# Kernel optimization log

Measured on AMD Instinct MI355X. Metric: run time of the kernel, lower is better.

Reference implementation:

```python
import jax, jax.numpy as jnp
import numpy as np

T, H, NH, NKV, HD, E, K, I = 1024, 2048, 16, 4, 128, 16, 2, 768
EPS = 1e-6
THETA = 10000.0


def setup_inputs() -> dict:
    key = jax.random.key(0)
    ks = jax.random.split(key, 8)
    s = 0.02
    return {
        "hidden_states": jax.random.normal(ks[0], (T, H), jnp.float32),
        "positions": jnp.arange(T, dtype=jnp.int32),
        "w_norm1": jnp.ones((H,), jnp.float32),
        "w_norm2": jnp.ones((H,), jnp.float32),
        "w_qkv": jax.random.normal(ks[1], (H, (NH + 2 * NKV) * HD), jnp.float32) * s,
        "w_qnorm": jnp.ones((HD,), jnp.float32),
        "w_knorm": jnp.ones((HD,), jnp.float32),
        "w_o": jax.random.normal(ks[2], (NH * HD, H), jnp.float32) * s,
        "w_router": jax.random.normal(ks[3], (H, E), jnp.float32) * s,
        "w_gate": jax.random.normal(ks[4], (E, H, I), jnp.float32) * s,
        "w_up": jax.random.normal(ks[5], (E, H, I), jnp.float32) * s,
        "w_down": jax.random.normal(ks[6], (E, I, H), jnp.float32) * s,
    }


def rmsnorm(x, w):
    return x * jax.lax.rsqrt(jnp.mean(x * x, axis=-1, keepdims=True) + EPS) * w


def apply_rope(x, positions):
    # NEOX-style rotary, full head_dim. x: [T, n_heads, HD]
    half = HD // 2
    inv_freq = 1.0 / (THETA ** (jnp.arange(half, dtype=jnp.float32) / half))
    ang = positions.astype(jnp.float32)[:, None] * inv_freq  # [T, half]
    cos = jnp.cos(ang)[:, None, :]
    sin = jnp.sin(ang)[:, None, :]
    x1, x2 = x[..., :half], x[..., half:]
    return jnp.concatenate([x1 * cos - x2 * sin, x2 * cos + x1 * sin], axis=-1)


def reference(hidden_states, positions, w_norm1, w_norm2, w_qkv, w_qnorm, w_knorm,
              w_o, w_router, w_gate, w_up, w_down):
    # prepare_attn: residual = x; h = input_layernorm(x)
    residual = hidden_states
    h = rmsnorm(hidden_states, w_norm1)

    # --- attention (bidirectional, GQA, per-head q/k RMSNorm + RoPE) ---
    qkv = h @ w_qkv
    q, k, v = jnp.split(qkv, [NH * HD, NH * HD + NKV * HD], axis=-1)
    q = rmsnorm(q.reshape(T, NH, HD), w_qnorm)
    k = rmsnorm(k.reshape(T, NKV, HD), w_knorm)
    v = v.reshape(T, NKV, HD)
    q = apply_rope(q, positions)
    k = apply_rope(k, positions)
    rep = NH // NKV
    kf = jnp.repeat(k, rep, axis=1)  # [T, NH, HD]
    vf = jnp.repeat(v, rep, axis=1)
    scores = jnp.einsum('tnd,snd->nts', q, kf) * (HD ** -0.5)  # [NH, T, T]
    p = jax.nn.softmax(scores, axis=-1)
    ctx = jnp.einsum('nts,snd->tnd', p, vf).reshape(T, NH * HD)
    attn_out = ctx @ w_o

    # prepare_mlp: residual = residual + attn_out; h = post_attention_layernorm(residual)
    residual = residual + attn_out
    h = rmsnorm(residual, w_norm2)

    # --- sparse MoE: softmax router, top-k renormalize, SwiGLU experts ---
    logits = h @ w_router
    probs = jax.nn.softmax(logits, axis=-1)
    topw, topi = jax.lax.top_k(probs, K)
    topw = topw / jnp.sum(topw, axis=-1, keepdims=True)
    gates = jnp.zeros((T, E), h.dtype).at[jnp.arange(T)[:, None], topi].set(topw)
    g = jnp.einsum('th,ehi->eti', h, w_gate)
    u = jnp.einsum('th,ehi->eti', h, w_up)
    y = jnp.einsum('eti,eih->eth', jax.nn.silu(g) * u, w_down)
    moe_out = jnp.einsum('eth,te->th', y, gates)

    return moe_out, residual
```

## Files before the change

### kernel.cpp

```cpp
#include <hip/hip_runtime.h>

#define T_    1024
#define H_    2048
#define NH_   16
#define NKV_  4
#define HD_   128
#define E_    16
#define I_    768
#define QKVN  3072

typedef __attribute__((ext_vector_type(8))) short  short8;
typedef __attribute__((ext_vector_type(4))) float  f32x4;
typedef unsigned short u16;

#define LDP 40

__device__ inline u16 f2bf(float f) {
  unsigned u = __builtin_bit_cast(unsigned, f);
  return (u16)((u + 0x7fffu + ((u >> 16) & 1u)) >> 16);
}
__device__ inline float bf2f(u16 h) {
  unsigned u = ((unsigned)h) << 16;
  return __builtin_bit_cast(float, u);
}

__device__ inline float blk_sum(float v, float* lds) {
#pragma unroll
  for (int o = 32; o; o >>= 1) v += __shfl_down(v, o);
  int w = threadIdx.x >> 6;
  __syncthreads();
  if ((threadIdx.x & 63) == 0) lds[w] = v;
  __syncthreads();
  float s = lds[0];
  int nw = blockDim.x >> 6;
  for (int i = 1; i < nw; ++i) s += lds[i];
  return s;
}
__device__ inline float blk_max(float v, float* lds) {
#pragma unroll
  for (int o = 32; o; o >>= 1) v = fmaxf(v, __shfl_down(v, o));
  int w = threadIdx.x >> 6;
  __syncthreads();
  if ((threadIdx.x & 63) == 0) lds[w] = v;
  __syncthreads();
  float s = lds[0];
  int nw = blockDim.x >> 6;
  for (int i = 1; i < nw; ++i) s = fmaxf(s, lds[i]);
  return s;
}


struct AU4 { uint4 v; };
struct BU2 { uint2 v; };
struct F4  { float v[4]; };

__device__ inline void wrS(u16* lds, const AU4& r) {
  *(uint4*)(lds + (threadIdx.x >> 2) * LDP + (threadIdx.x & 3) * 8) = r.v;
}
__device__ inline void wrS(u16* lds, const BU2& r) {
  *(uint2*)(lds + (threadIdx.x >> 3) * LDP + (threadIdx.x & 7) * 4) = r.v;
}
__device__ inline void wrS(u16* lds, const F4& r) {
  int n = threadIdx.x & 63, kh = (threadIdx.x >> 6) * 4;
  uint2 w;
  w.x = (unsigned)f2bf(r.v[0]) | ((unsigned)f2bf(r.v[1]) << 16);
  w.y = (unsigned)f2bf(r.v[2]) | ((unsigned)f2bf(r.v[3]) << 16);
  *(uint2*)(lds + n * LDP + kh) = w;
}

__device__ inline void mma2(const u16* As, const u16* Bs, f32x4 acc[2][2]) {
  const int lane = threadIdx.x & 63, wv = threadIdx.x >> 6;
  const int wr = wv >> 1, wc = wv & 1;
  const int kk = (lane >> 4) * 8, rr = lane & 15;
  short8 aF[2], bF[2];
#pragma unroll
  for (int m = 0; m < 2; ++m)
    aF[m] = *(const short8*)(As + (wr * 32 + m * 16 + rr) * LDP + kk);
#pragma unroll
  for (int n = 0; n < 2; ++n)
    bF[n] = *(const short8*)(Bs + (wc * 32 + n * 16 + rr) * LDP + kk);
#pragma unroll
  for (int m = 0; m < 2; ++m)
#pragma unroll
    for (int n = 0; n < 2; ++n)
      acc[m][n] = __builtin_amdgcn_mfma_f32_16x16x32_bf16(aF[m], bF[n], acc[m][n], 0, 0, 0);
}

#define ZERO_ACC(acc) do { \
  _Pragma("unroll") for (int m_ = 0; m_ < 2; ++m_) \
  _Pragma("unroll") for (int n_ = 0; n_ < 2; ++n_) acc[m_][n_] = (f32x4){0.f,0.f,0.f,0.f}; \
} while (0)

#define EPI_ROW(m, r)  (((threadIdx.x >> 6) >> 1) * 32 + (m)*16 + (((threadIdx.x&63) >> 4) * 4) + (r))
#define EPI_COL(n)     ((((threadIdx.x >> 6) & 1) * 32) + (n)*16 + ((threadIdx.x&63) & 15))

template<int NT, class AT, class BT, class LA, class LB>
__device__ inline void pipe2(LA la, LB lb, u16* A0, u16* B0, u16* A1, u16* B1,
                             f32x4 acc[2][2]) {
  AT a0, a1; BT b0, b1;
  la(a0, 0); lb(b0, 0);
  la(a1, 1); lb(b1, 1);
  wrS(A0, a0); wrS(B0, b0);
  if (NT > 2) { la(a0, 2); lb(b0, 2); }
#pragma unroll 1
  for (int kt = 0; kt < NT; kt += 2) {
    __syncthreads();
    wrS(A1, a1); wrS(B1, b1);
    if (kt + 3 < NT) { la(a1, kt + 3); lb(b1, kt + 3); }
    mma2(A0, B0, acc);
    __syncthreads();
    if (kt + 2 < NT) { wrS(A0, a0); wrS(B0, b0); }
    if (kt + 4 < NT) { la(a0, kt + 4); lb(b0, kt + 4); }
    mma2(A1, B1, acc);
  }
}


__global__ __launch_bounds__(256) void k_rms1(const float* x, const float* w, u16* out) {
  __shared__ float lds[4];
  int t = blockIdx.x, tid = threadIdx.x;
  float v[8]; float ss = 0.f;
#pragma unroll
  for (int i = 0; i < 8; ++i) { v[i] = x[(size_t)t * H_ + tid + 256 * i]; ss += v[i] * v[i]; }
  ss = blk_sum(ss, lds);
  float inv = rsqrtf(ss * (1.f / H_) + 1e-6f);
#pragma unroll
  for (int i = 0; i < 8; ++i)
    out[(size_t)t * H_ + tid + 256 * i] = f2bf(v[i] * inv * w[tid + 256 * i]);
}

__global__ __launch_bounds__(256) void k_rms2(const float* x, const float* w,
                                              float* outf, u16* outb) {
  __shared__ float lds[4];
  int t = blockIdx.x, tid = threadIdx.x;
  float v[8]; float ss = 0.f;
#pragma unroll
  for (int i = 0; i < 8; ++i) { v[i] = x[(size_t)t * H_ + tid + 256 * i]; ss += v[i] * v[i]; }
  ss = blk_sum(ss, lds);
  float inv = rsqrtf(ss * (1.f / H_) + 1e-6f);
#pragma unroll
  for (int i = 0; i < 8; ++i) {
    float r = v[i] * inv * w[tid + 256 * i];
    outf[(size_t)t * H_ + tid + 256 * i] = r;
    outb[(size_t)t * H_ + tid + 256 * i] = f2bf(r);
  }
}

__global__ __launch_bounds__(512) void k_qkv(const u16* h1, const float* wqkv, float* qkv) {
  __shared__ __align__(16) u16 A0[128 * LDP], B0[64 * LDP], A1[128 * LDP], B1[64 * LDP];
  int bn = blockIdx.x, bm = blockIdx.y;
  f32x4 acc[2][2]; ZERO_ACC(acc);
  auto la = [&](AU4& r, int kt) {
    r.v = *(const uint4*)(h1 + (size_t)(bm * 128 + (threadIdx.x >> 2)) * H_ + kt * 32 + (threadIdx.x & 3) * 8);
  };
  auto lb = [&](F4& r, int kt) {
    int n = threadIdx.x & 63, kh = (threadIdx.x >> 6) * 4;
    const float* src = wqkv + (size_t)(kt * 32 + kh) * QKVN + bn * 64 + n;
#pragma unroll
    for (int j = 0; j < 4; ++j) r.v[j] = src[(size_t)j * QKVN];
  };
  pipe2<H_ / 32, AU4, F4>(la, lb, A0, B0, A1, B1, acc);
#pragma unroll
  for (int m = 0; m < 2; ++m)
#pragma unroll
    for (int n = 0; n < 2; ++n) {
      f32x4 a = acc[m][n];
#pragma unroll
      for (int r = 0; r < 4; ++r)
        qkv[(size_t)(bm * 128 + EPI_ROW(m, r)) * QKVN + bn * 64 + EPI_COL(n)] = a[r];
    }
}

__global__ __launch_bounds__(256) void k_qkrope(const float* qkv, const int* pos,
                                                const float* wq, const float* wk,
                                                u16* q, u16* kk, u16* vT) {
  __shared__ float cs[64], sn[64];
  int t = blockIdx.x, tid = threadIdx.x, lane = tid & 63, w = tid >> 6;
  if (tid < 64) {
    float fr = expf(-((float)tid / 64.f) * 9.210340371976184f);
    float ang = (float)pos[t] * fr;
    float s_, c_; sincosf(ang, &s_, &c_);
    cs[tid] = c_; sn[tid] = s_;
  }
  __syncthreads();
  const float* row = qkv + (size_t)t * QKVN;
  for (int h = w; h < NH_; h += 4) {
    float x1 = row[h * 128 + lane], x2 = row[h * 128 + 64 + lane];
    float ss = x1 * x1 + x2 * x2;
#pragma unroll
    for (int o = 32; o; o >>= 1) ss += __shfl_down(ss, o);
    ss = __shfl(ss, 0);
    float inv = rsqrtf(ss * (1.f / HD_) + 1e-6f);
    float n1 = x1 * inv * wq[lane], n2 = x2 * inv * wq[64 + lane];
    float o1 = n1 * cs[lane] - n2 * sn[lane];
    float o2 = n2 * cs[lane] + n1 * sn[lane];
    q[(size_t)t * (NH_ * HD_) + h * 128 + lane] = f2bf(o1);
    q[(size_t)t * (NH_ * HD_) + h * 128 + 64 + lane] = f2bf(o2);
  }
  if (w < NKV_) {
    int h = w;
    float x1 = row[2048 + h * 128 + lane], x2 = row[2048 + h * 128 + 64 + lane];
    float ss = x1 * x1 + x2 * x2;
#pragma unroll
    for (int o = 32; o; o >>= 1) ss += __shfl_down(ss, o);
    ss = __shfl(ss, 0);
    float inv = rsqrtf(ss * (1.f / HD_) + 1e-6f);
    float n1 = x1 * inv * wk[lane], n2 = x2 * inv * wk[64 + lane];
    float o1 = n1 * cs[lane] - n2 * sn[lane];
    float o2 = n2 * cs[lane] + n1 * sn[lane];
    kk[((size_t)h * T_ + t) * HD_ + lane] = f2bf(o1);
    kk[((size_t)h * T_ + t) * HD_ + 64 + lane] = f2bf(o2);
    float v1 = row[2560 + h * 128 + lane], v2 = row[2560 + h * 128 + 64 + lane];
    vT[((size_t)(h * 128 + lane)) * T_ + t] = f2bf(v1);
    vT[((size_t)(h * 128 + 64 + lane)) * T_ + t] = f2bf(v2);
  }
}

__global__ __launch_bounds__(512) void k_scores(const u16* q, const u16* kb, u16* S) {
  __shared__ __align__(16) u16 A0[128 * LDP], B0[64 * LDP], A1[128 * LDP], B1[64 * LDP];
  int h = blockIdx.x, sn = blockIdx.y, qm = blockIdx.z;
  const u16* Aq = q + h * 128;
  const u16* Bk = kb + (size_t)(h >> 2) * T_ * HD_;
  f32x4 acc[2][2]; ZERO_ACC(acc);
  auto la = [&](AU4& r, int kt) {
    r.v = *(const uint4*)(Aq + (size_t)(qm * 128 + (threadIdx.x >> 2)) * (NH_ * HD_) + kt * 32 + (threadIdx.x & 3) * 8);
  };
  auto lb = [&](BU2& r, int kt) {
    r.v = *(const uint2*)(Bk + (size_t)(sn * 64 + (threadIdx.x >> 3)) * HD_ + kt * 32 + (threadIdx.x & 7) * 4);
  };
  pipe2<HD_ / 32, AU4, BU2>(la, lb, A0, B0, A1, B1, acc);
  const float scale = 0.08838834764831845f;
#pragma unroll
  for (int m = 0; m < 2; ++m)
#pragma unroll
    for (int n = 0; n < 2; ++n) {
      f32x4 a = acc[m][n];
#pragma unroll
      for (int r = 0; r < 4; ++r)
        S[((size_t)h * T_ + qm * 128 + EPI_ROW(m, r)) * T_ + sn * 64 + EPI_COL(n)] =
            f2bf(a[r] * scale);
    }
}

__global__ __launch_bounds__(256) void k_softmax(u16* S) {
  __shared__ float lds[4];
  int t = blockIdx.x, h = blockIdx.y, tid = threadIdx.x;
  u16* rowp = S + ((size_t)h * T_ + t) * T_;
  float x[4];
#pragma unroll
  for (int i = 0; i < 4; ++i) x[i] = bf2f(rowp[tid + 256 * i]);
  float m = fmaxf(fmaxf(x[0], x[1]), fmaxf(x[2], x[3]));
  m = blk_max(m, lds);
  float s = 0.f;
#pragma unroll
  for (int i = 0; i < 4; ++i) { x[i] = __expf(x[i] - m); s += x[i]; }
  s = blk_sum(s, lds);
  float inv = 1.f / s;
#pragma unroll
  for (int i = 0; i < 4; ++i) rowp[tid + 256 * i] = f2bf(x[i] * inv);
}

__global__ __launch_bounds__(512) void k_pv(const u16* P, const u16* vT, u16* ctx) {
  __shared__ __align__(16) u16 A0[128 * LDP], B0[64 * LDP], A1[128 * LDP], B1[64 * LDP];
  int h = blockIdx.x, qm = blockIdx.y, nb = blockIdx.z;
  const u16* Ap = P + (size_t)h * T_ * T_;
  const u16* Bv = vT + (size_t)(h >> 2) * HD_ * T_ + (size_t)nb * 64 * T_;
  f32x4 acc[2][2]; ZERO_ACC(acc);
  auto la = [&](AU4& r, int kt) {
    r.v = *(const uint4*)(Ap + (size_t)(qm * 128 + (threadIdx.x >> 2)) * T_ + kt * 32 + (threadIdx.x & 3) * 8);
  };
  auto lb = [&](BU2& r, int kt) {
    r.v = *(const uint2*)(Bv + (size_t)(threadIdx.x >> 3) * T_ + kt * 32 + (threadIdx.x & 7) * 4);
  };
  pipe2<T_ / 32, AU4, BU2>(la, lb, A0, B0, A1, B1, acc);
#pragma unroll
  for (int m = 0; m < 2; ++m)
#pragma unroll
    for (int n = 0; n < 2; ++n) {
      f32x4 a = acc[m][n];
#pragma unroll
      for (int r = 0; r < 4; ++r)
        ctx[(size_t)(qm * 128 + EPI_ROW(m, r)) * (NH_ * HD_) + h * 128 + nb * 64 + EPI_COL(n)] =
            f2bf(a[r]);
    }
}

__global__ __launch_bounds__(512) void k_wo(const u16* ctx, const float* wo,
                                            const float* hs, float* resid) {
  __shared__ __align__(16) u16 A0[128 * LDP], B0[64 * LDP], A1[128 * LDP], B1[64 * LDP];
  int bn = blockIdx.x, bm = blockIdx.y;
  f32x4 acc[2][2]; ZERO_ACC(acc);
  auto la = [&](AU4& r, int kt) {
    r.v = *(const uint4*)(ctx + (size_t)(bm * 128 + (threadIdx.x >> 2)) * H_ + kt * 32 + (threadIdx.x & 3) * 8);
  };
  auto lb = [&](F4& r, int kt) {
    int n = threadIdx.x & 63, kh = (threadIdx.x >> 6) * 4;
    const float* src = wo + (size_t)(kt * 32 + kh) * H_ + bn * 64 + n;
#pragma unroll
    for (int j = 0; j < 4; ++j) r.v[j] = src[(size_t)j * H_];
  };
  pipe2<H_ / 32, AU4, F4>(la, lb, A0, B0, A1, B1, acc);
#pragma unroll
  for (int m = 0; m < 2; ++m)
#pragma unroll
    for (int n = 0; n < 2; ++n) {
      f32x4 a = acc[m][n];
#pragma unroll
      for (int r = 0; r < 4; ++r) {
        size_t idx = (size_t)(bm * 128 + EPI_ROW(m, r)) * H_ + bn * 64 + EPI_COL(n);
        resid[idx] = a[r] + hs[idx];
      }
    }
}

__global__ __launch_bounds__(256) void k_router(const float* h2f, const float* wr_,
                                                int* topi, float* topw, int* cnt) {
  __shared__ float xs[H_];
  __shared__ float red[4][16];
  __shared__ float lg[16];
  int t = blockIdx.x, tid = threadIdx.x;
#pragma unroll
  for (int i = 0; i < 8; ++i) xs[tid + 256 * i] = h2f[(size_t)t * H_ + tid + 256 * i];
  __syncthreads();
  int e = tid & 15, p = tid >> 4;
  float s = 0.f;
  int b0 = p * 128;
  for (int i = 0; i < 128; ++i) s += xs[b0 + i] * wr_[(size_t)(b0 + i) * E_ + e];
  s += __shfl_down(s, 32);
  s += __shfl_down(s, 16);
  int lane = tid & 63, w = tid >> 6;
  if (lane < 16) red[w][lane] = s;
  __syncthreads();
  if (tid < 16) lg[tid] = red[0][tid] + red[1][tid] + red[2][tid] + red[3][tid];
  __syncthreads();
  if (tid == 0) {
    float l1 = -1e30f; int e1 = 0;
    for (int i = 0; i < E_; ++i) if (lg[i] > l1) { l1 = lg[i]; e1 = i; }
    float l2 = -1e30f; int e2 = 0;
    for (int i = 0; i < E_; ++i) if (i != e1 && lg[i] > l2) { l2 = lg[i]; e2 = i; }
    float d = __expf(l2 - l1);
    float w1 = 1.f / (1.f + d), w2 = d / (1.f + d);
    topi[2 * t] = e1; topi[2 * t + 1] = e2;
    topw[2 * t] = w1; topw[2 * t + 1] = w2;
    atomicAdd(&cnt[e1], 1);
    atomicAdd(&cnt[e2], 1);
  }
}

__global__ void k_scan(const int* cnt, int* basearr) {
  if (threadIdx.x == 0) {
    int b = 0;
    for (int e = 0; e < E_; ++e) { basearr[e] = b; b += cnt[e]; }
    basearr[E_] = b;
  }
}

__global__ __launch_bounds__(256) void k_assign(const int* topi, const float* topw,
                                                const int* basearr, int* posc,
                                                int* tok, float* wslot) {
  int t = blockIdx.x * 256 + threadIdx.x;
  if (t < T_) {
#pragma unroll
    for (int j = 0; j < 2; ++j) {
      int e = topi[2 * t + j];
      int p = atomicAdd(&posc[e], 1);
      int s = basearr[e] + p;
      tok[s] = t;
      wslot[s] = topw[2 * t + j];
    }
  }
}

__global__ __launch_bounds__(512) void k_gateup(const u16* h2b,
                                                const float* wg, const float* wu,
                                                const int* cnt, const int* basearr, const int* tok,
                                                u16* act) {
  __shared__ __align__(16) u16 A0[128 * LDP], B0[64 * LDP], A1[128 * LDP], B1[64 * LDP];
  __shared__ int gat_s[128];
  int e = blockIdx.x;
  int c = cnt[e];
  int mt = blockIdx.z;
  if (mt * 128 >= c) return;
  int basee = basearr[e];
  int gmax = c - mt * 128;
  int n0 = blockIdx.y * 32;
  int tid = threadIdx.x;
  if (tid < 128) {
    int r = mt * 128 + tid;
    gat_s[tid] = (r < c) ? tok[basee + r] : tok[basee];
  }
  __syncthreads();
  const float* Bg = wg + (size_t)e * H_ * I_;
  const float* Bu = wu + (size_t)e * H_ * I_;
  f32x4 acc[2][2]; ZERO_ACC(acc);
  auto la = [&](AU4& r, int kt) {
    r.v = *(const uint4*)(h2b + (size_t)gat_s[threadIdx.x >> 2] * H_ + kt * 32 + (threadIdx.x & 3) * 8);
  };
  auto lb = [&](F4& r, int kt) {
    int cidx = threadIdx.x & 63, kh = (threadIdx.x >> 6) * 4;
    int fn = cidx >> 4;
    const float* base = (fn & 1) ? Bu : Bg;
    int col = n0 + (fn >> 1) * 16 + (cidx & 15);
    const float* src = base + (size_t)(kt * 32 + kh) * I_ + col;
#pragma unroll
    for (int j = 0; j < 4; ++j) r.v[j] = src[(size_t)j * I_];
  };
  pipe2<H_ / 32, AU4, F4>(la, lb, A0, B0, A1, B1, acc);
  int slot0 = basee + mt * 128;
  int col = n0 + ((threadIdx.x >> 6) & 1) * 16 + ((threadIdx.x & 63) & 15);
#pragma unroll
  for (int m = 0; m < 2; ++m) {
#pragma unroll
    for (int r = 0; r < 4; ++r) {
      int row = EPI_ROW(m, r);
      if (row >= gmax) continue;
      float g = acc[m][0][r], u = acc[m][1][r];
      float sg = g / (1.f + __expf(-g));
      act[(size_t)(slot0 + row) * I_ + col] = f2bf(sg * u);
    }
  }
}

__global__ __launch_bounds__(512) void k_down(const u16* act, const float* wd,
                                              const int* cnt, const int* basearr,
                                              const int* tok, const float* wslot,
                                              float* moe) {
  __shared__ __align__(16) u16 A0[128 * LDP], B0[64 * LDP], A1[128 * LDP], B1[64 * LDP];
  int e = blockIdx.y;
  int c = cnt[e];
  int mt = blockIdx.z;
  if (mt * 128 >= c) return;
  int basee = basearr[e];
  int gmax = c - mt * 128;
  int slot0 = basee + mt * 128;
  int n0 = blockIdx.x * 64;
  const u16* Ap = act + (size_t)slot0 * I_;
  const float* Bp = wd + (size_t)e * I_ * H_;
  f32x4 acc[2][2]; ZERO_ACC(acc);
  auto la = [&](AU4& r, int kt) {
    r.v = *(const uint4*)(Ap + (size_t)(threadIdx.x >> 2) * I_ + kt * 32 + (threadIdx.x & 3) * 8);
  };
  auto lb = [&](F4& r, int kt) {
    int n = threadIdx.x & 63, kh = (threadIdx.x >> 6) * 4;
    const float* src = Bp + (size_t)(kt * 32 + kh) * H_ + n0 + n;
#pragma unroll
    for (int j = 0; j < 4; ++j) r.v[j] = src[(size_t)j * H_];
  };
  pipe2<I_ / 32, AU4, F4>(la, lb, A0, B0, A1, B1, acc);
#pragma unroll
  for (int m = 0; m < 2; ++m)
#pragma unroll
    for (int n = 0; n < 2; ++n) {
      f32x4 a = acc[m][n];
#pragma unroll
      for (int r = 0; r < 4; ++r) {
        int row = EPI_ROW(m, r);
        if (row >= gmax) continue;
        int col = EPI_COL(n);
        int slot = slot0 + row;
        float wgt = wslot[slot];
        int tk = tok[slot];
        atomicAdd(&moe[(size_t)tk * H_ + n0 + col], a[r] * wgt);
      }
    }
}

extern "C" void kernel_launch(void* const* d_in, const int* in_sizes, int n_in,
                              void* d_out, int out_size, void* d_ws, size_t ws_size,
                              hipStream_t stream) {
  const float* hs    = (const float*)d_in[0];
  const int*   pos   = (const int*)d_in[1];
  const float* wn1   = (const float*)d_in[2];
  const float* wn2   = (const float*)d_in[3];
  const float* wqkv  = (const float*)d_in[4];
  const float* wqn   = (const float*)d_in[5];
  const float* wkn   = (const float*)d_in[6];
  const float* wo    = (const float*)d_in[7];
  const float* wrt   = (const float*)d_in[8];
  const float* wg    = (const float*)d_in[9];
  const float* wu    = (const float*)d_in[10];
  const float* wd    = (const float*)d_in[11];
  float* out = (float*)d_out;
  float* moe_out = out;
  float* resid   = out + (size_t)T_ * H_;

  char* ws = (char*)d_ws;
  size_t off = 0;
  auto alloc = [&](size_t bytes) { size_t r = off; off = (off + bytes + 255) & ~(size_t)255; return r; };
  u16*   h1   = (u16*)  (ws + alloc((size_t)T_ * H_ * 2));
  float* qkv  = (float*)(ws + alloc((size_t)T_ * QKVN * 4));
  u16*   q    = (u16*)  (ws + alloc((size_t)T_ * NH_ * HD_ * 2));
  u16*   kb   = (u16*)  (ws + alloc((size_t)NKV_ * T_ * HD_ * 2));
  u16*   vT   = (u16*)  (ws + alloc((size_t)NKV_ * HD_ * T_ * 2));
  u16*   S    = (u16*)  (ws + alloc((size_t)NH_ * T_ * T_ * 2));
  u16*   ctx  = (u16*)  (ws + alloc((size_t)T_ * NH_ * HD_ * 2));
  float* h2f  = (float*)(ws + alloc((size_t)T_ * H_ * 4));
  u16*   h2b  = (u16*)  (ws + alloc((size_t)T_ * H_ * 2));
  u16*   act  = (u16*)  (ws + alloc((size_t)(2 * T_ + 256) * I_ * 2));
  int*   topi = (int*)  (ws + alloc((size_t)T_ * 2 * 4));
  float* topw = (float*)(ws + alloc((size_t)T_ * 2 * 4));
  int*   cnt  = (int*)  (ws + alloc(32 * 4));
  int*   posc = cnt + 16;
  int*   base = (int*)  (ws + alloc(32 * 4));
  int*   tok  = (int*)  (ws + alloc((size_t)(2 * T_ + 128) * 4));
  float* wsl  = (float*)(ws + alloc((size_t)(2 * T_ + 128) * 4));
  (void)ws_size; (void)in_sizes; (void)n_in; (void)out_size;

  hipMemsetAsync(moe_out, 0, (size_t)T_ * H_ * 4, stream);
  hipMemsetAsync(cnt, 0, 32 * 4, stream);

  k_rms1<<<T_, 256, 0, stream>>>(hs, wn1, h1);
  k_qkv<<<dim3(QKVN / 64, T_ / 128), 512, 0, stream>>>(h1, wqkv, qkv);
  k_qkrope<<<T_, 256, 0, stream>>>(qkv, pos, wqn, wkn, q, kb, vT);
  k_scores<<<dim3(NH_, T_ / 64, T_ / 128), 512, 0, stream>>>(q, kb, S);
  k_softmax<<<dim3(T_, NH_), 256, 0, stream>>>(S);
  k_pv<<<dim3(NH_, T_ / 128, HD_ / 64), 512, 0, stream>>>(S, vT, ctx);
  k_wo<<<dim3(H_ / 64, T_ / 128), 512, 0, stream>>>(ctx, wo, hs, resid);
  k_rms2<<<T_, 256, 0, stream>>>(resid, wn2, h2f, h2b);
  k_router<<<T_, 256, 0, stream>>>(h2f, wrt, topi, topw, cnt);
  k_scan<<<1, 64, 0, stream>>>(cnt, base);
  k_assign<<<4, 256, 0, stream>>>(topi, topw, base, posc, tok, wsl);
  k_gateup<<<dim3(E_, I_ / 32, T_ / 128), 512, 0, stream>>>(h2b, wg, wu, cnt, base, tok, act);
  k_down<<<dim3(H_ / 64, E_, T_ / 128), 512, 0, stream>>>(act, wd, cnt, base, tok, wsl, moe_out);
}
```

Before: 341.5 us.

## Load GEMM operand tiles directly into LDS and shrink tiles to 64 rows

Every MFMA GEMM kernel now stages its bf16 A tile, and for attention also the B tile, with global_load_lds, writing straight from global memory into LDS instead of going through registers. The A tiles use an unpadded 32-element row stride to match the per-wave DMA layout. Block tiles shrink from 128x64 with 512 threads to 64x64 with 256 threads, and fp32 weight B loads now take 8 rows per thread. The aim is fewer register round trips and more blocks in flight. The cost is that fp32 weights are re-read by twice as many M tiles, and the unpadded LDS layout may cause bank conflicts.

```diff
diff --git a/kernel.cpp b/kernel.cpp
--- a/kernel.cpp
+++ b/kernel.cpp
@@ -13,7 +13,8 @@
 typedef __attribute__((ext_vector_type(4))) float  f32x4;
 typedef unsigned short u16;
 
-#define LDP 40
+#define LDPA 32
+#define LDPB 40
 
 __device__ inline u16 f2bf(float f) {
   unsigned u = __builtin_bit_cast(unsigned, f);
@@ -22,6 +23,12 @@
 __device__ inline float bf2f(u16 h) {
   unsigned u = ((unsigned)h) << 16;
   return __builtin_bit_cast(float, u);
+}
+
+__device__ inline void gll16(const u16* g, u16* l) {
+  __builtin_amdgcn_global_load_lds(
+      (const __attribute__((address_space(1))) void*)g,
+      (__attribute__((address_space(3))) void*)l, 16, 0, 0);
 }
 
 __device__ inline float blk_sum(float v, float* lds) {
@@ -50,24 +57,19 @@
 }
 
 
-struct AU4 { uint4 v; };
-struct BU2 { uint2 v; };
-struct F4  { float v[4]; };
-
-__device__ inline void wrS(u16* lds, const AU4& r) {
-  *(uint4*)(lds + (threadIdx.x >> 2) * LDP + (threadIdx.x & 3) * 8) = r.v;
-}
-__device__ inline void wrS(u16* lds, const BU2& r) {
-  *(uint2*)(lds + (threadIdx.x >> 3) * LDP + (threadIdx.x & 7) * 4) = r.v;
-}
-__device__ inline void wrS(u16* lds, const F4& r) {
-  int n = threadIdx.x & 63, kh = (threadIdx.x >> 6) * 4;
-  uint2 w;
+struct F8 { float v[8]; };
+
+__device__ inline void wrB(u16* lds, const F8& r) {
+  int n = threadIdx.x & 63, kh = (threadIdx.x >> 6) * 8;
+  uint4 w;
   w.x = (unsigned)f2bf(r.v[0]) | ((unsigned)f2bf(r.v[1]) << 16);
   w.y = (unsigned)f2bf(r.v[2]) | ((unsigned)f2bf(r.v[3]) << 16);
-  *(uint2*)(lds + n * LDP + kh) = w;
-}
-
+  w.z = (unsigned)f2bf(r.v[4]) | ((unsigned)f2bf(r.v[5]) << 16);
+  w.w = (unsigned)f2bf(r.v[6]) | ((unsigned)f2bf(r.v[7]) << 16);
+  *(uint4*)(lds + n * LDPB + kh) = w;
+}
+
+template<int SA, int SB>
 __device__ inline void mma2(const u16* As, const u16* Bs, f32x4 acc[2][2]) {
   const int lane = threadIdx.x & 63, wv = threadIdx.x >> 6;
   const int wr = wv >> 1, wc = wv & 1;
@@ -75,10 +77,10 @@
   short8 aF[2], bF[2];
 #pragma unroll
   for (int m = 0; m < 2; ++m)
-    aF[m] = *(const short8*)(As + (wr * 32 + m * 16 + rr) * LDP + kk);
+    aF[m] = *(const short8*)(As + (wr * 32 + m * 16 + rr) * SA + kk);
 #pragma unroll
   for (int n = 0; n < 2; ++n)
-    bF[n] = *(const short8*)(Bs + (wc * 32 + n * 16 + rr) * LDP + kk);
+    bF[n] = *(const short8*)(Bs + (wc * 32 + n * 16 + rr) * SB + kk);
 #pragma unroll
   for (int m = 0; m < 2; ++m)
 #pragma unroll
@@ -94,24 +96,40 @@
 #define EPI_ROW(m, r)  (((threadIdx.x >> 6) >> 1) * 32 + (m)*16 + (((threadIdx.x&63) >> 4) * 4) + (r))
 #define EPI_COL(n)     ((((threadIdx.x >> 6) & 1) * 32) + (n)*16 + ((threadIdx.x&63) & 15))
 
-template<int NT, class AT, class BT, class LA, class LB>
-__device__ inline void pipe2(LA la, LB lb, u16* A0, u16* B0, u16* A1, u16* B1,
+template<int NT, class GA, class LB>
+__device__ inline void pipeF(GA gllA, LB ldB, u16* A0, u16* B0, u16* A1, u16* B1,
                              f32x4 acc[2][2]) {
-  AT a0, a1; BT b0, b1;
-  la(a0, 0); lb(b0, 0);
-  la(a1, 1); lb(b1, 1);
-  wrS(A0, a0); wrS(B0, b0);
-  if (NT > 2) { la(a0, 2); lb(b0, 2); }
+  F8 b0, b1;
+  gllA(A0, 0);
+  ldB(b0, 0); ldB(b1, 1);
+  wrB(B0, b0);
+  if (NT > 2) ldB(b0, 2);
 #pragma unroll 1
   for (int kt = 0; kt < NT; kt += 2) {
     __syncthreads();
-    wrS(A1, a1); wrS(B1, b1);
-    if (kt + 3 < NT) { la(a1, kt + 3); lb(b1, kt + 3); }
-    mma2(A0, B0, acc);
+    gllA(A1, kt + 1);
+    wrB(B1, b1);
+    if (kt + 3 < NT) ldB(b1, kt + 3);
+    mma2<LDPA, LDPB>(A0, B0, acc);
     __syncthreads();
-    if (kt + 2 < NT) { wrS(A0, a0); wrS(B0, b0); }
-    if (kt + 4 < NT) { la(a0, kt + 4); lb(b0, kt + 4); }
-    mma2(A1, B1, acc);
+    if (kt + 2 < NT) { gllA(A0, kt + 2); wrB(B0, b0); }
+    if (kt + 4 < NT) ldB(b0, kt + 4);
+    mma2<LDPA, LDPB>(A1, B1, acc);
+  }
+}
+
+template<int NT, class GA, class GB>
+__device__ inline void pipeG(GA gllA, GB gllB, u16* A0, u16* B0, u16* A1, u16* B1,
+                             f32x4 acc[2][2]) {
+  gllA(A0, 0); gllB(B0, 0);
+#pragma unroll 1
+  for (int kt = 0; kt < NT; kt += 2) {
+    __syncthreads();
+    gllA(A1, kt + 1); gllB(B1, kt + 1);
+    mma2<LDPA, LDPA>(A0, B0, acc);
+    __syncthreads();
+    if (kt + 2 < NT) { gllA(A0, kt + 2); gllB(B0, kt + 2); }
+    mma2<LDPA, LDPA>(A1, B1, acc);
   }
 }
 
@@ -146,20 +164,22 @@
   }
 }
 
-__global__ __launch_bounds__(512) void k_qkv(const u16* h1, const float* wqkv, float* qkv) {
-  __shared__ __align__(16) u16 A0[128 * LDP], B0[64 * LDP], A1[128 * LDP], B1[64 * LDP];
+__global__ __launch_bounds__(256) void k_qkv(const u16* h1, const float* wqkv, float* qkv) {
+  __shared__ __align__(16) u16 A0[64 * LDPA], A1[64 * LDPA];
+  __shared__ __align__(16) u16 B0[64 * LDPB], B1[64 * LDPB];
   int bn = blockIdx.x, bm = blockIdx.y;
   f32x4 acc[2][2]; ZERO_ACC(acc);
-  auto la = [&](AU4& r, int kt) {
-    r.v = *(const uint4*)(h1 + (size_t)(bm * 128 + (threadIdx.x >> 2)) * H_ + kt * 32 + (threadIdx.x & 3) * 8);
-  };
-  auto lb = [&](F4& r, int kt) {
-    int n = threadIdx.x & 63, kh = (threadIdx.x >> 6) * 4;
+  auto la = [&](u16* As, int kt) {
+    gll16(h1 + (size_t)(bm * 64 + (threadIdx.x >> 2)) * H_ + kt * 32 + (threadIdx.x & 3) * 8,
+          As + (threadIdx.x & 192) * 8);
+  };
+  auto lb = [&](F8& r, int kt) {
+    int n = threadIdx.x & 63, kh = (threadIdx.x >> 6) * 8;
     const float* src = wqkv + (size_t)(kt * 32 + kh) * QKVN + bn * 64 + n;
 #pragma unroll
-    for (int j = 0; j < 4; ++j) r.v[j] = src[(size_t)j * QKVN];
-  };
-  pipe2<H_ / 32, AU4, F4>(la, lb, A0, B0, A1, B1, acc);
+    for (int j = 0; j < 8; ++j) r.v[j] = src[(size_t)j * QKVN];
+  };
+  pipeF<H_ / 32>(la, lb, A0, B0, A1, B1, acc);
 #pragma unroll
   for (int m = 0; m < 2; ++m)
 #pragma unroll
@@ -167,7 +187,7 @@
       f32x4 a = acc[m][n];
 #pragma unroll
       for (int r = 0; r < 4; ++r)
-        qkv[(size_t)(bm * 128 + EPI_ROW(m, r)) * QKVN + bn * 64 + EPI_COL(n)] = a[r];
+        qkv[(size_t)(bm * 64 + EPI_ROW(m, r)) * QKVN + bn * 64 + EPI_COL(n)] = a[r];
     }
 }
 
@@ -216,19 +236,22 @@
   }
 }
 
-__global__ __launch_bounds__(512) void k_scores(const u16* q, const u16* kb, u16* S) {
-  __shared__ __align__(16) u16 A0[128 * LDP], B0[64 * LDP], A1[128 * LDP], B1[64 * LDP];
+__global__ __launch_bounds__(256) void k_scores(const u16* q, const u16* kb, u16* S) {
+  __shared__ __align__(16) u16 A0[64 * LDPA], A1[64 * LDPA];
+  __shared__ __align__(16) u16 B0[64 * LDPA], B1[64 * LDPA];
   int h = blockIdx.x, sn = blockIdx.y, qm = blockIdx.z;
   const u16* Aq = q + h * 128;
   const u16* Bk = kb + (size_t)(h >> 2) * T_ * HD_;
   f32x4 acc[2][2]; ZERO_ACC(acc);
-  auto la = [&](AU4& r, int kt) {
-    r.v = *(const uint4*)(Aq + (size_t)(qm * 128 + (threadIdx.x >> 2)) * (NH_ * HD_) + kt * 32 + (threadIdx.x & 3) * 8);
-  };
-  auto lb = [&](BU2& r, int kt) {
-    r.v = *(const uint2*)(Bk + (size_t)(sn * 64 + (threadIdx.x >> 3)) * HD_ + kt * 32 + (threadIdx.x & 7) * 4);
-  };
-  pipe2<HD_ / 32, AU4, BU2>(la, lb, A0, B0, A1, B1, acc);
+  auto la = [&](u16* As, int kt) {
+    gll16(Aq + (size_t)(qm * 64 + (threadIdx.x >> 2)) * (NH_ * HD_) + kt * 32 + (threadIdx.x & 3) * 8,
+          As + (threadIdx.x & 192) * 8);
+  };
+  auto lb = [&](u16* Bs, int kt) {
+    gll16(Bk + (size_t)(sn * 64 + (threadIdx.x >> 2)) * HD_ + kt * 32 + (threadIdx.x & 3) * 8,
+          Bs + (threadIdx.x & 192) * 8);
+  };
+  pipeG<HD_ / 32>(la, lb, A0, B0, A1, B1, acc);
   const float scale = 0.08838834764831845f;
 #pragma unroll
   for (int m = 0; m < 2; ++m)
@@ -237,7 +260,7 @@
       f32x4 a = acc[m][n];
 #pragma unroll
       for (int r = 0; r < 4; ++r)
-        S[((size_t)h * T_ + qm * 128 + EPI_ROW(m, r)) * T_ + sn * 64 + EPI_COL(n)] =
+        S[((size_t)h * T_ + qm * 64 + EPI_ROW(m, r)) * T_ + sn * 64 + EPI_COL(n)] =
             f2bf(a[r] * scale);
     }
 }
@@ -260,19 +283,22 @@
   for (int i = 0; i < 4; ++i) rowp[tid + 256 * i] = f2bf(x[i] * inv);
 }
 
-__global__ __launch_bounds__(512) void k_pv(const u16* P, const u16* vT, u16* ctx) {
-  __shared__ __align__(16) u16 A0[128 * LDP], B0[64 * LDP], A1[128 * LDP], B1[64 * LDP];
+__global__ __launch_bounds__(256) void k_pv(const u16* P, const u16* vT, u16* ctx) {
+  __shared__ __align__(16) u16 A0[64 * LDPA], A1[64 * LDPA];
+  __shared__ __align__(16) u16 B0[64 * LDPA], B1[64 * LDPA];
   int h = blockIdx.x, qm = blockIdx.y, nb = blockIdx.z;
   const u16* Ap = P + (size_t)h * T_ * T_;
   const u16* Bv = vT + (size_t)(h >> 2) * HD_ * T_ + (size_t)nb * 64 * T_;
   f32x4 acc[2][2]; ZERO_ACC(acc);
-  auto la = [&](AU4& r, int kt) {
-    r.v = *(const uint4*)(Ap + (size_t)(qm * 128 + (threadIdx.x >> 2)) * T_ + kt * 32 + (threadIdx.x & 3) * 8);
-  };
-  auto lb = [&](BU2& r, int kt) {
-    r.v = *(const uint2*)(Bv + (size_t)(threadIdx.x >> 3) * T_ + kt * 32 + (threadIdx.x & 7) * 4);
-  };
-  pipe2<T_ / 32, AU4, BU2>(la, lb, A0, B0, A1, B1, acc);
+  auto la = [&](u16* As, int kt) {
+    gll16(Ap + (size_t)(qm * 64 + (threadIdx.x >> 2)) * T_ + kt * 32 + (threadIdx.x & 3) * 8,
+          As + (threadIdx.x & 192) * 8);
+  };
+  auto lb = [&](u16* Bs, int kt) {
+    gll16(Bv + (size_t)(threadIdx.x >> 2) * T_ + kt * 32 + (threadIdx.x & 3) * 8,
+          Bs + (threadIdx.x & 192) * 8);
+  };
+  pipeG<T_ / 32>(la, lb, A0, B0, A1, B1, acc);
 #pragma unroll
   for (int m = 0; m < 2; ++m)
 #pragma unroll
@@ -280,26 +306,28 @@
       f32x4 a = acc[m][n];
 #pragma unroll
       for (int r = 0; r < 4; ++r)
-        ctx[(size_t)(qm * 128 + EPI_ROW(m, r)) * (NH_ * HD_) + h * 128 + nb * 64 + EPI_COL(n)] =
+        ctx[(size_t)(qm * 64 + EPI_ROW(m, r)) * (NH_ * HD_) + h * 128 + nb * 64 + EPI_COL(n)] =
             f2bf(a[r]);
     }
 }
 
-__global__ __launch_bounds__(512) void k_wo(const u16* ctx, const float* wo,
+__global__ __launch_bounds__(256) void k_wo(const u16* ctx, const float* wo,
                                             const float* hs, float* resid) {
-  __shared__ __align__(16) u16 A0[128 * LDP], B0[64 * LDP], A1[128 * LDP], B1[64 * LDP];
+  __shared__ __align__(16) u16 A0[64 * LDPA], A1[64 * LDPA];
+  __shared__ __align__(16) u16 B0[64 * LDPB], B1[64 * LDPB];
   int bn = blockIdx.x, bm = blockIdx.y;
   f32x4 acc[2][2]; ZERO_ACC(acc);
-  auto la = [&](AU4& r, int kt) {
-    r.v = *(const uint4*)(ctx + (size_t)(bm * 128 + (threadIdx.x >> 2)) * H_ + kt * 32 + (threadIdx.x & 3) * 8);
-  };
-  auto lb = [&](F4& r, int kt) {
-    int n = threadIdx.x & 63, kh = (threadIdx.x >> 6) * 4;
+  auto la = [&](u16* As, int kt) {
+    gll16(ctx + (size_t)(bm * 64 + (threadIdx.x >> 2)) * H_ + kt * 32 + (threadIdx.x & 3) * 8,
+          As + (threadIdx.x & 192) * 8);
+  };
+  auto lb = [&](F8& r, int kt) {
+    int n = threadIdx.x & 63, kh = (threadIdx.x >> 6) * 8;
     const float* src = wo + (size_t)(kt * 32 + kh) * H_ + bn * 64 + n;
 #pragma unroll
-    for (int j = 0; j < 4; ++j) r.v[j] = src[(size_t)j * H_];
-  };
-  pipe2<H_ / 32, AU4, F4>(la, lb, A0, B0, A1, B1, acc);
+    for (int j = 0; j < 8; ++j) r.v[j] = src[(size_t)j * H_];
+  };
+  pipeF<H_ / 32>(la, lb, A0, B0, A1, B1, acc);
 #pragma unroll
   for (int m = 0; m < 2; ++m)
 #pragma unroll
@@ -307,7 +335,7 @@
       f32x4 a = acc[m][n];
 #pragma unroll
       for (int r = 0; r < 4; ++r) {
-        size_t idx = (size_t)(bm * 128 + EPI_ROW(m, r)) * H_ + bn * 64 + EPI_COL(n);
+        size_t idx = (size_t)(bm * 64 + EPI_ROW(m, r)) * H_ + bn * 64 + EPI_COL(n);
         resid[idx] = a[r] + hs[idx];
       }
     }
@@ -371,43 +399,45 @@
   }
 }
 
-__global__ __launch_bounds__(512) void k_gateup(const u16* h2b,
+__global__ __launch_bounds__(256) void k_gateup(const u16* h2b,
                                                 const float* wg, const float* wu,
                                                 const int* cnt, const int* basearr, const int* tok,
                                                 u16* act) {
-  __shared__ __align__(16) u16 A0[128 * LDP], B0[64 * LDP], A1[128 * LDP], B1[64 * LDP];
-  __shared__ int gat_s[128];
+  __shared__ __align__(16) u16 A0[64 * LDPA], A1[64 * LDPA];
+  __shared__ __align__(16) u16 B0[64 * LDPB], B1[64 * LDPB];
+  __shared__ int gat_s[64];
   int e = blockIdx.x;
   int c = cnt[e];
   int mt = blockIdx.z;
-  if (mt * 128 >= c) return;
+  if (mt * 64 >= c) return;
   int basee = basearr[e];
-  int gmax = c - mt * 128;
+  int gmax = c - mt * 64;
   int n0 = blockIdx.y * 32;
   int tid = threadIdx.x;
-  if (tid < 128) {
-    int r = mt * 128 + tid;
+  if (tid < 64) {
+    int r = mt * 64 + tid;
     gat_s[tid] = (r < c) ? tok[basee + r] : tok[basee];
   }
   __syncthreads();
+  int grow = gat_s[tid >> 2];
   const float* Bg = wg + (size_t)e * H_ * I_;
   const float* Bu = wu + (size_t)e * H_ * I_;
   f32x4 acc[2][2]; ZERO_ACC(acc);
-  auto la = [&](AU4& r, int kt) {
-    r.v = *(const uint4*)(h2b + (size_t)gat_s[threadIdx.x >> 2] * H_ + kt * 32 + (threadIdx.x & 3) * 8);
-  };
-  auto lb = [&](F4& r, int kt) {
-    int cidx = threadIdx.x & 63, kh = (threadIdx.x >> 6) * 4;
+  auto la = [&](u16* As, int kt) {
+    gll16(h2b + (size_t)grow * H_ + kt * 32 + (tid & 3) * 8, As + (tid & 192) * 8);
+  };
+  auto lb = [&](F8& r, int kt) {
+    int cidx = tid & 63, kh = (tid >> 6) * 8;
     int fn = cidx >> 4;
     const float* base = (fn & 1) ? Bu : Bg;
     int col = n0 + (fn >> 1) * 16 + (cidx & 15);
     const float* src = base + (size_t)(kt * 32 + kh) * I_ + col;
 #pragma unroll
-    for (int j = 0; j < 4; ++j) r.v[j] = src[(size_t)j * I_];
-  };
-  pipe2<H_ / 32, AU4, F4>(la, lb, A0, B0, A1, B1, acc);
-  int slot0 = basee + mt * 128;
-  int col = n0 + ((threadIdx.x >> 6) & 1) * 16 + ((threadIdx.x & 63) & 15);
+    for (int j = 0; j < 8; ++j) r.v[j] = src[(size_t)j * I_];
+  };
+  pipeF<H_ / 32>(la, lb, A0, B0, A1, B1, acc);
+  int slot0 = basee + mt * 64;
+  int col = n0 + ((tid >> 6) & 1) * 16 + ((tid & 63) & 15);
 #pragma unroll
   for (int m = 0; m < 2; ++m) {
 #pragma unroll
@@ -421,32 +451,34 @@
   }
 }
 
-__global__ __launch_bounds__(512) void k_down(const u16* act, const float* wd,
+__global__ __launch_bounds__(256) void k_down(const u16* act, const float* wd,
                                               const int* cnt, const int* basearr,
                                               const int* tok, const float* wslot,
                                               float* moe) {
-  __shared__ __align__(16) u16 A0[128 * LDP], B0[64 * LDP], A1[128 * LDP], B1[64 * LDP];
+  __shared__ __align__(16) u16 A0[64 * LDPA], A1[64 * LDPA];
+  __shared__ __align__(16) u16 B0[64 * LDPB], B1[64 * LDPB];
   int e = blockIdx.y;
   int c = cnt[e];
   int mt = blockIdx.z;
-  if (mt * 128 >= c) return;
+  if (mt * 64 >= c) return;
   int basee = basearr[e];
-  int gmax = c - mt * 128;
-  int slot0 = basee + mt * 128;
+  int gmax = c - mt * 64;
+  int slot0 = basee + mt * 64;
   int n0 = blockIdx.x * 64;
   const u16* Ap = act + (size_t)slot0 * I_;
   const float* Bp = wd + (size_t)e * I_ * H_;
   f32x4 acc[2][2]; ZERO_ACC(acc);
-  auto la = [&](AU4& r, int kt) {
-    r.v = *(const uint4*)(Ap + (size_t)(threadIdx.x >> 2) * I_ + kt * 32 + (threadIdx.x & 3) * 8);
-  };
-  auto lb = [&](F4& r, int kt) {
-    int n = threadIdx.x & 63, kh = (threadIdx.x >> 6) * 4;
+  auto la = [&](u16* As, int kt) {
+    gll16(Ap + (size_t)(threadIdx.x >> 2) * I_ + kt * 32 + (threadIdx.x & 3) * 8,
+          As + (threadIdx.x & 192) * 8);
+  };
+  auto lb = [&](F8& r, int kt) {
+    int n = threadIdx.x & 63, kh = (threadIdx.x >> 6) * 8;
     const float* src = Bp + (size_t)(kt * 32 + kh) * H_ + n0 + n;
 #pragma unroll
-    for (int j = 0; j < 4; ++j) r.v[j] = src[(size_t)j * H_];
-  };
-  pipe2<I_ / 32, AU4, F4>(la, lb, A0, B0, A1, B1, acc);
+    for (int j = 0; j < 8; ++j) r.v[j] = src[(size_t)j * H_];
+  };
+  pipeF<I_ / 32>(la, lb, A0, B0, A1, B1, acc);
 #pragma unroll
   for (int m = 0; m < 2; ++m)
 #pragma unroll
@@ -510,16 +542,16 @@
   hipMemsetAsync(cnt, 0, 32 * 4, stream);
 
   k_rms1<<<T_, 256, 0, stream>>>(hs, wn1, h1);
-  k_qkv<<<dim3(QKVN / 64, T_ / 128), 512, 0, stream>>>(h1, wqkv, qkv);
+  k_qkv<<<dim3(QKVN / 64, T_ / 64), 256, 0, stream>>>(h1, wqkv, qkv);
   k_qkrope<<<T_, 256, 0, stream>>>(qkv, pos, wqn, wkn, q, kb, vT);
-  k_scores<<<dim3(NH_, T_ / 64, T_ / 128), 512, 0, stream>>>(q, kb, S);
+  k_scores<<<dim3(NH_, T_ / 64, T_ / 64), 256, 0, stream>>>(q, kb, S);
   k_softmax<<<dim3(T_, NH_), 256, 0, stream>>>(S);
-  k_pv<<<dim3(NH_, T_ / 128, HD_ / 64), 512, 0, stream>>>(S, vT, ctx);
-  k_wo<<<dim3(H_ / 64, T_ / 128), 512, 0, stream>>>(ctx, wo, hs, resid);
+  k_pv<<<dim3(NH_, T_ / 64, HD_ / 64), 256, 0, stream>>>(S, vT, ctx);
+  k_wo<<<dim3(H_ / 64, T_ / 64), 256, 0, stream>>>(ctx, wo, hs, resid);
   k_rms2<<<T_, 256, 0, stream>>>(resid, wn2, h2f, h2b);
   k_router<<<T_, 256, 0, stream>>>(h2f, wrt, topi, topw, cnt);
   k_scan<<<1, 64, 0, stream>>>(cnt, base);
   k_assign<<<4, 256, 0, stream>>>(topi, topw, base, posc, tok, wsl);
-  k_gateup<<<dim3(E_, I_ / 32, T_ / 128), 512, 0, stream>>>(h2b, wg, wu, cnt, base, tok, act);
-  k_down<<<dim3(H_ / 64, E_, T_ / 128), 512, 0, stream>>>(act, wd, cnt, base, tok, wsl, moe_out);
-}
+  k_gateup<<<dim3(E_, I_ / 32, T_ / 64), 256, 0, stream>>>(h2b, wg, wu, cnt, base, tok, act);
+  k_down<<<dim3(H_ / 64, E_, T_ / 64), 256, 0, stream>>>(act, wd, cnt, base, tok, wsl, moe_out);
+}
```

After: 360.7 us. +5.6%, slower.

## Split-K the QKV, O-proj, gate/up and down GEMMs with atomic accumulation

Applied to the files above, without the earlier changes.

Splits the K dimension in two for the QKV, Wo, gate/up and down projection GEMMs, doubling the grid and accumulating partial results with float atomicAdd into zeroed buffers. The residual add is replaced by pre-copying hidden_states into the output, and the SiLU*up epilogue moves into a separate k_silu kernel over fp32 partial buffers. The aim is more blocks to fill the GPU's compute units, since the base grids are small (e.g. 384 or 256 blocks). The cost is extra memsets, atomic traffic, larger fp32 intermediates and one extra launch.

```diff
diff --git a/kernel.cpp b/kernel.cpp
--- a/kernel.cpp
+++ b/kernel.cpp
@@ -148,18 +148,20 @@
 
 __global__ __launch_bounds__(512) void k_qkv(const u16* h1, const float* wqkv, float* qkv) {
   __shared__ __align__(16) u16 A0[128 * LDP], B0[64 * LDP], A1[128 * LDP], B1[64 * LDP];
-  int bn = blockIdx.x, bm = blockIdx.y;
+  int bn = blockIdx.x, bm = blockIdx.y, ks = blockIdx.z;
+  const u16* Ab = h1 + ks * (H_ / 2);
+  const float* Bb = wqkv + (size_t)ks * (H_ / 2) * QKVN;
   f32x4 acc[2][2]; ZERO_ACC(acc);
   auto la = [&](AU4& r, int kt) {
-    r.v = *(const uint4*)(h1 + (size_t)(bm * 128 + (threadIdx.x >> 2)) * H_ + kt * 32 + (threadIdx.x & 3) * 8);
+    r.v = *(const uint4*)(Ab + (size_t)(bm * 128 + (threadIdx.x >> 2)) * H_ + kt * 32 + (threadIdx.x & 3) * 8);
   };
   auto lb = [&](F4& r, int kt) {
     int n = threadIdx.x & 63, kh = (threadIdx.x >> 6) * 4;
-    const float* src = wqkv + (size_t)(kt * 32 + kh) * QKVN + bn * 64 + n;
+    const float* src = Bb + (size_t)(kt * 32 + kh) * QKVN + bn * 64 + n;
 #pragma unroll
     for (int j = 0; j < 4; ++j) r.v[j] = src[(size_t)j * QKVN];
   };
-  pipe2<H_ / 32, AU4, F4>(la, lb, A0, B0, A1, B1, acc);
+  pipe2<H_ / 64, AU4, F4>(la, lb, A0, B0, A1, B1, acc);
 #pragma unroll
   for (int m = 0; m < 2; ++m)
 #pragma unroll
@@ -167,7 +169,7 @@
       f32x4 a = acc[m][n];
 #pragma unroll
       for (int r = 0; r < 4; ++r)
-        qkv[(size_t)(bm * 128 + EPI_ROW(m, r)) * QKVN + bn * 64 + EPI_COL(n)] = a[r];
+        atomicAdd(&qkv[(size_t)(bm * 128 + EPI_ROW(m, r)) * QKVN + bn * 64 + EPI_COL(n)], a[r]);
     }
 }
 
@@ -285,31 +287,30 @@
     }
 }
 
-__global__ __launch_bounds__(512) void k_wo(const u16* ctx, const float* wo,
-                                            const float* hs, float* resid) {
+__global__ __launch_bounds__(512) void k_wo(const u16* ctx, const float* wo, float* resid) {
   __shared__ __align__(16) u16 A0[128 * LDP], B0[64 * LDP], A1[128 * LDP], B1[64 * LDP];
-  int bn = blockIdx.x, bm = blockIdx.y;
+  int bn = blockIdx.x, bm = blockIdx.y, ks = blockIdx.z;
+  const u16* Ab = ctx + ks * (H_ / 2);
+  const float* Bb = wo + (size_t)ks * (H_ / 2) * H_;
   f32x4 acc[2][2]; ZERO_ACC(acc);
   auto la = [&](AU4& r, int kt) {
-    r.v = *(const uint4*)(ctx + (size_t)(bm * 128 + (threadIdx.x >> 2)) * H_ + kt * 32 + (threadIdx.x & 3) * 8);
+    r.v = *(const uint4*)(Ab + (size_t)(bm * 128 + (threadIdx.x >> 2)) * H_ + kt * 32 + (threadIdx.x & 3) * 8);
   };
   auto lb = [&](F4& r, int kt) {
     int n = threadIdx.x & 63, kh = (threadIdx.x >> 6) * 4;
-    const float* src = wo + (size_t)(kt * 32 + kh) * H_ + bn * 64 + n;
+    const float* src = Bb + (size_t)(kt * 32 + kh) * H_ + bn * 64 + n;
 #pragma unroll
     for (int j = 0; j < 4; ++j) r.v[j] = src[(size_t)j * H_];
   };
-  pipe2<H_ / 32, AU4, F4>(la, lb, A0, B0, A1, B1, acc);
+  pipe2<H_ / 64, AU4, F4>(la, lb, A0, B0, A1, B1, acc);
 #pragma unroll
   for (int m = 0; m < 2; ++m)
 #pragma unroll
     for (int n = 0; n < 2; ++n) {
       f32x4 a = acc[m][n];
 #pragma unroll
-      for (int r = 0; r < 4; ++r) {
-        size_t idx = (size_t)(bm * 128 + EPI_ROW(m, r)) * H_ + bn * 64 + EPI_COL(n);
-        resid[idx] = a[r] + hs[idx];
-      }
+      for (int r = 0; r < 4; ++r)
+        atomicAdd(&resid[(size_t)(bm * 128 + EPI_ROW(m, r)) * H_ + bn * 64 + EPI_COL(n)], a[r]);
     }
 }
 
@@ -374,12 +375,12 @@
 __global__ __launch_bounds__(512) void k_gateup(const u16* h2b,
                                                 const float* wg, const float* wu,
                                                 const int* cnt, const int* basearr, const int* tok,
-                                                u16* act) {
+                                                float* gpart, float* upart) {
   __shared__ __align__(16) u16 A0[128 * LDP], B0[64 * LDP], A1[128 * LDP], B1[64 * LDP];
   __shared__ int gat_s[128];
   int e = blockIdx.x;
   int c = cnt[e];
-  int mt = blockIdx.z;
+  int mt = blockIdx.z >> 1, ks = blockIdx.z & 1;
   if (mt * 128 >= c) return;
   int basee = basearr[e];
   int gmax = c - mt * 128;
@@ -390,11 +391,12 @@
     gat_s[tid] = (r < c) ? tok[basee + r] : tok[basee];
   }
   __syncthreads();
-  const float* Bg = wg + (size_t)e * H_ * I_;
-  const float* Bu = wu + (size_t)e * H_ * I_;
+  const u16* Ab = h2b + ks * (H_ / 2);
+  const float* Bg = wg + (size_t)e * H_ * I_ + (size_t)ks * (H_ / 2) * I_;
+  const float* Bu = wu + (size_t)e * H_ * I_ + (size_t)ks * (H_ / 2) * I_;
   f32x4 acc[2][2]; ZERO_ACC(acc);
   auto la = [&](AU4& r, int kt) {
-    r.v = *(const uint4*)(h2b + (size_t)gat_s[threadIdx.x >> 2] * H_ + kt * 32 + (threadIdx.x & 3) * 8);
+    r.v = *(const uint4*)(Ab + (size_t)gat_s[threadIdx.x >> 2] * H_ + kt * 32 + (threadIdx.x & 3) * 8);
   };
   auto lb = [&](F4& r, int kt) {
     int cidx = threadIdx.x & 63, kh = (threadIdx.x >> 6) * 4;
@@ -405,7 +407,7 @@
 #pragma unroll
     for (int j = 0; j < 4; ++j) r.v[j] = src[(size_t)j * I_];
   };
-  pipe2<H_ / 32, AU4, F4>(la, lb, A0, B0, A1, B1, acc);
+  pipe2<H_ / 64, AU4, F4>(la, lb, A0, B0, A1, B1, acc);
   int slot0 = basee + mt * 128;
   int col = n0 + ((threadIdx.x >> 6) & 1) * 16 + ((threadIdx.x & 63) & 15);
 #pragma unroll
@@ -414,11 +416,25 @@
     for (int r = 0; r < 4; ++r) {
       int row = EPI_ROW(m, r);
       if (row >= gmax) continue;
-      float g = acc[m][0][r], u = acc[m][1][r];
-      float sg = g / (1.f + __expf(-g));
-      act[(size_t)(slot0 + row) * I_ + col] = f2bf(sg * u);
-    }
-  }
+      size_t idx = (size_t)(slot0 + row) * I_ + col;
+      atomicAdd(&gpart[idx], acc[m][0][r]);
+      atomicAdd(&upart[idx], acc[m][1][r]);
+    }
+  }
+}
+
+__global__ __launch_bounds__(256) void k_silu(const float* gpart, const float* upart, u16* act) {
+  int gid = blockIdx.x * 256 + threadIdx.x;
+  float4 g = ((const float4*)gpart)[gid];
+  float4 u = ((const float4*)upart)[gid];
+  float o0 = g.x / (1.f + __expf(-g.x)) * u.x;
+  float o1 = g.y / (1.f + __expf(-g.y)) * u.y;
+  float o2 = g.z / (1.f + __expf(-g.z)) * u.z;
+  float o3 = g.w / (1.f + __expf(-g.w)) * u.w;
+  uint2 w;
+  w.x = (unsigned)f2bf(o0) | ((unsigned)f2bf(o1) << 16);
+  w.y = (unsigned)f2bf(o2) | ((unsigned)f2bf(o3) << 16);
+  ((uint2*)act)[gid] = w;
 }
 
 __global__ __launch_bounds__(512) void k_down(const u16* act, const float* wd,
@@ -428,14 +444,14 @@
   __shared__ __align__(16) u16 A0[128 * LDP], B0[64 * LDP], A1[128 * LDP], B1[64 * LDP];
   int e = blockIdx.y;
   int c = cnt[e];
-  int mt = blockIdx.z;
+  int mt = blockIdx.z >> 1, ks = blockIdx.z & 1;
   if (mt * 128 >= c) return;
   int basee = basearr[e];
   int gmax = c - mt * 128;
   int slot0 = basee + mt * 128;
   int n0 = blockIdx.x * 64;
-  const u16* Ap = act + (size_t)slot0 * I_;
-  const float* Bp = wd + (size_t)e * I_ * H_;
+  const u16* Ap = act + (size_t)slot0 * I_ + ks * (I_ / 2);
+  const float* Bp = wd + (size_t)e * I_ * H_ + (size_t)ks * (I_ / 2) * H_;
   f32x4 acc[2][2]; ZERO_ACC(acc);
   auto la = [&](AU4& r, int kt) {
     r.v = *(const uint4*)(Ap + (size_t)(threadIdx.x >> 2) * I_ + kt * 32 + (threadIdx.x & 3) * 8);
@@ -446,7 +462,7 @@
 #pragma unroll
     for (int j = 0; j < 4; ++j) r.v[j] = src[(size_t)j * H_];
   };
-  pipe2<I_ / 32, AU4, F4>(la, lb, A0, B0, A1, B1, acc);
+  pipe2<I_ / 64, AU4, F4>(la, lb, A0, B0, A1, B1, acc);
 #pragma unroll
   for (int m = 0; m < 2; ++m)
 #pragma unroll
@@ -487,39 +503,46 @@
   char* ws = (char*)d_ws;
   size_t off = 0;
   auto alloc = [&](size_t bytes) { size_t r = off; off = (off + bytes + 255) & ~(size_t)255; return r; };
-  u16*   h1   = (u16*)  (ws + alloc((size_t)T_ * H_ * 2));
-  float* qkv  = (float*)(ws + alloc((size_t)T_ * QKVN * 4));
-  u16*   q    = (u16*)  (ws + alloc((size_t)T_ * NH_ * HD_ * 2));
-  u16*   kb   = (u16*)  (ws + alloc((size_t)NKV_ * T_ * HD_ * 2));
-  u16*   vT   = (u16*)  (ws + alloc((size_t)NKV_ * HD_ * T_ * 2));
-  u16*   S    = (u16*)  (ws + alloc((size_t)NH_ * T_ * T_ * 2));
-  u16*   ctx  = (u16*)  (ws + alloc((size_t)T_ * NH_ * HD_ * 2));
-  float* h2f  = (float*)(ws + alloc((size_t)T_ * H_ * 4));
-  u16*   h2b  = (u16*)  (ws + alloc((size_t)T_ * H_ * 2));
-  u16*   act  = (u16*)  (ws + alloc((size_t)(2 * T_ + 256) * I_ * 2));
-  int*   topi = (int*)  (ws + alloc((size_t)T_ * 2 * 4));
-  float* topw = (float*)(ws + alloc((size_t)T_ * 2 * 4));
-  int*   cnt  = (int*)  (ws + alloc(32 * 4));
-  int*   posc = cnt + 16;
-  int*   base = (int*)  (ws + alloc(32 * 4));
-  int*   tok  = (int*)  (ws + alloc((size_t)(2 * T_ + 128) * 4));
-  float* wsl  = (float*)(ws + alloc((size_t)(2 * T_ + 128) * 4));
+  u16*   h1    = (u16*)  (ws + alloc((size_t)T_ * H_ * 2));
+  float* qkv   = (float*)(ws + alloc((size_t)T_ * QKVN * 4));
+  u16*   q     = (u16*)  (ws + alloc((size_t)T_ * NH_ * HD_ * 2));
+  u16*   kb    = (u16*)  (ws + alloc((size_t)NKV_ * T_ * HD_ * 2));
+  u16*   vT    = (u16*)  (ws + alloc((size_t)NKV_ * HD_ * T_ * 2));
+  u16*   S     = (u16*)  (ws + alloc((size_t)NH_ * T_ * T_ * 2));
+  u16*   ctx   = (u16*)  (ws + alloc((size_t)T_ * NH_ * HD_ * 2));
+  float* h2f   = (float*)(ws + alloc((size_t)T_ * H_ * 4));
+  u16*   h2b   = (u16*)  (ws + alloc((size_t)T_ * H_ * 2));
+  u16*   act   = (u16*)  (ws + alloc((size_t)(2 * T_ + 256) * I_ * 2));
+  float* gpart = (float*)(ws + alloc((size_t)2 * T_ * I_ * 4));
+  float* upart = (float*)(ws + alloc((size_t)2 * T_ * I_ * 4));
+  int*   topi  = (int*)  (ws + alloc((size_t)T_ * 2 * 4));
+  float* topw  = (float*)(ws + alloc((size_t)T_ * 2 * 4));
+  int*   cnt   = (int*)  (ws + alloc(32 * 4));
+  int*   posc  = cnt + 16;
+  int*   base  = (int*)  (ws + alloc(32 * 4));
+  int*   tok   = (int*)  (ws + alloc((size_t)(2 * T_ + 128) * 4));
+  float* wsl   = (float*)(ws + alloc((size_t)(2 * T_ + 128) * 4));
   (void)ws_size; (void)in_sizes; (void)n_in; (void)out_size;
 
   hipMemsetAsync(moe_out, 0, (size_t)T_ * H_ * 4, stream);
   hipMemsetAsync(cnt, 0, 32 * 4, stream);
+  hipMemsetAsync(qkv, 0, (size_t)T_ * QKVN * 4, stream);
+  hipMemsetAsync(gpart, 0, (size_t)2 * T_ * I_ * 4, stream);
+  hipMemsetAsync(upart, 0, (size_t)2 * T_ * I_ * 4, stream);
+  hipMemcpyAsync(resid, hs, (size_t)T_ * H_ * 4, hipMemcpyDeviceToDevice, stream);
 
   k_rms1<<<T_, 256, 0, stream>>>(hs, wn1, h1);
-  k_qkv<<<dim3(QKVN / 64, T_ / 128), 512, 0, stream>>>(h1, wqkv, qkv);
+  k_qkv<<<dim3(QKVN / 64, T_ / 128, 2), 512, 0, stream>>>(h1, wqkv, qkv);
   k_qkrope<<<T_, 256, 0, stream>>>(qkv, pos, wqn, wkn, q, kb, vT);
   k_scores<<<dim3(NH_, T_ / 64, T_ / 128), 512, 0, stream>>>(q, kb, S);
   k_softmax<<<dim3(T_, NH_), 256, 0, stream>>>(S);
   k_pv<<<dim3(NH_, T_ / 128, HD_ / 64), 512, 0, stream>>>(S, vT, ctx);
-  k_wo<<<dim3(H_ / 64, T_ / 128), 512, 0, stream>>>(ctx, wo, hs, resid);
+  k_wo<<<dim3(H_ / 64, T_ / 128, 2), 512, 0, stream>>>(ctx, wo, resid);
   k_rms2<<<T_, 256, 0, stream>>>(resid, wn2, h2f, h2b);
   k_router<<<T_, 256, 0, stream>>>(h2f, wrt, topi, topw, cnt);
   k_scan<<<1, 64, 0, stream>>>(cnt, base);
   k_assign<<<4, 256, 0, stream>>>(topi, topw, base, posc, tok, wsl);
-  k_gateup<<<dim3(E_, I_ / 32, T_ / 128), 512, 0, stream>>>(h2b, wg, wu, cnt, base, tok, act);
-  k_down<<<dim3(H_ / 64, E_, T_ / 128), 512, 0, stream>>>(act, wd, cnt, base, tok, wsl, moe_out);
-}
+  k_gateup<<<dim3(E_, I_ / 32, 2 * T_ / 128), 512, 0, stream>>>(h2b, wg, wu, cnt, base, tok, gpart, upart);
+  k_silu<<<(2 * T_ * I_) / 1024, 256, 0, stream>>>(gpart, upart, act);
+  k_down<<<dim3(H_ / 64, E_, 2 * T_ / 128), 512, 0, stream>>>(act, wd, cnt, base, tok, wsl, moe_out);
+}
```

Result: slower. 369.9 us (+8.3%).
